# Kernel optimization log

Hardware: AMD Instinct MI355X
Metric: run time of the kernel (lower is better)

Reference implementation:

```python
import jax, jax.numpy as jnp
import numpy as np
from jax import lax

D_MODEL = 1000
D_INNER = 2000   # expand=2
D_STATE = 8
D_CONV = 4
DT_RANK = 63     # ceil(1000/16)
DIM_OUT = 64


def setup_inputs() -> dict:
    key = jax.random.key(0)
    ks = jax.random.split(key, 16)
    s = 0.02
    x = jax.random.normal(ks[0], (8, 2048, D_MODEL), dtype=jnp.float32)
    params = {
        'w_norm': jnp.ones((D_MODEL,), jnp.float32),
        'W_in':   jax.random.normal(ks[1], (D_MODEL, 2 * D_INNER)) * s,
        'conv_w': jax.random.normal(ks[2], (D_INNER, D_CONV)) * s,
        'conv_b': jnp.zeros((D_INNER,), jnp.float32),
        'W_xproj': jax.random.normal(ks[3], (D_INNER, DT_RANK + 2 * D_STATE)) * s,
        'W_dt':   jax.random.normal(ks[4], (DT_RANK, D_INNER)) * s,
        'b_dt':   jax.random.normal(ks[5], (D_INNER,)) * s,
        'A_log':  jnp.broadcast_to(jnp.log(jnp.arange(1, D_STATE + 1, dtype=jnp.float32)), (D_INNER, D_STATE)).copy(),
        'Dp':     jnp.ones((D_INNER,), jnp.float32),
        'W_outp': jax.random.normal(ks[6], (D_INNER, D_MODEL)) * s,
        'W_fc':   jax.random.normal(ks[7], (D_MODEL, D_MODEL)) * s,
        'b_fc':   jnp.zeros((D_MODEL,), jnp.float32),
        'W_mu':   jax.random.normal(ks[8], (D_MODEL, DIM_OUT)) * s,
        'b_mu':   jnp.zeros((DIM_OUT,), jnp.float32),
        'W_sig':  jax.random.normal(ks[9], (D_MODEL, DIM_OUT)) * s,
        'b_sig':  jnp.zeros((DIM_OUT,), jnp.float32),
    }
    return {'x': x, **params}


def _rmsnorm(x, w, eps=1e-5):
    var = jnp.mean(x * x, axis=-1, keepdims=True)
    return x * lax.rsqrt(var + eps) * w


def _silu(x):
    return x * jax.nn.sigmoid(x)


def _mamba_block(x, w_norm, W_in, conv_w, conv_b, W_xproj, W_dt, b_dt, A_log, Dp, W_outp):
    B, L, _ = x.shape
    xn = _rmsnorm(x, w_norm)
    xz = xn @ W_in                                   # [B,L,2*ED]
    xc, z = jnp.split(xz, 2, axis=-1)                # each [B,L,ED]
    # depthwise causal conv1d
    xt = xc.transpose(0, 2, 1)                        # [B,ED,L]
    xt = lax.conv_general_dilated(
        xt, conv_w[:, None, :],                       # [ED,1,K]
        window_strides=(1,), padding=[(D_CONV - 1, 0)],
        feature_group_count=D_INNER,
        dimension_numbers=('NCH', 'OIH', 'NCH'))
    xc = xt.transpose(0, 2, 1) + conv_b               # [B,L,ED]
    xc = _silu(xc)
    dbc = xc @ W_xproj                                # [B,L,dt_rank+2N]
    dt, Bm, Cm = jnp.split(dbc, [DT_RANK, DT_RANK + D_STATE], axis=-1)
    delta = jax.nn.softplus(dt @ W_dt + b_dt)         # [B,L,ED]
    A = -jnp.exp(A_log)                               # [ED,N]

    def step(h, inp):
        x_t, d_t, B_t, C_t = inp                      # [B,ED],[B,ED],[B,N],[B,N]
        dA = jnp.exp(d_t[:, :, None] * A)             # [B,ED,N]
        h = dA * h + (d_t[:, :, None] * B_t[:, None, :]) * x_t[:, :, None]
        y = jnp.einsum('ben,bn->be', h, C_t)
        return h, y

    h0 = jnp.zeros((B, D_INNER, D_STATE), xc.dtype)
    xs = (xc.transpose(1, 0, 2), delta.transpose(1, 0, 2),
          Bm.transpose(1, 0, 2), Cm.transpose(1, 0, 2))
    _, ys = lax.scan(step, h0, xs)                    # [L,B,ED]
    y = ys.transpose(1, 0, 2) + Dp * xc               # [B,L,ED]
    y = y * _silu(z)
    return x + y @ W_outp                             # residual


def reference(x, w_norm, W_in, conv_w, conv_b, W_xproj, W_dt, b_dt, A_log, Dp,
              W_outp, W_fc, b_fc, W_mu, b_mu, W_sig, b_sig):
    e = _mamba_block(x, w_norm, W_in, conv_w, conv_b, W_xproj, W_dt, b_dt,
                     A_log, Dp, W_outp)
    e = e.mean(axis=1)                                # [B,d_model]; dropout=eval->identity
    h = jax.nn.elu(jnp.tanh(e @ W_fc + b_fc))
    mu = h @ W_mu + b_mu
    sigma = jax.nn.elu(h @ W_sig + b_sig) + 1.0 + 1e-14
    return (h, mu, sigma)
```

## Files before the change

kernel.cpp:

```cpp
#include <hip/hip_runtime.h>

#define DM    1000
#define DMP   1024
#define ED    2000
#define EDP   2048
#define NST   8
#define LSEQ  2048
#define NB    8
#define MTOT  16384
#define N1    4096
#define K1    1024
#define CHK   16
#define CLEN  (LSEQ/CHK)
#define MXCH  32

typedef unsigned short u16;
typedef __attribute__((ext_vector_type(4))) float f32x4;
typedef __attribute__((ext_vector_type(8))) short bf16x8;

__device__ __forceinline__ u16 f2bf(float f) {
    union { float f; unsigned u; } v; v.f = f;
    unsigned r = v.u + 0x7FFFu + ((v.u >> 16) & 1u);
    return (u16)(r >> 16);
}
__device__ __forceinline__ float bf2f(u16 h) {
    union { unsigned u; float f; } v; v.u = ((unsigned)h) << 16; return v.f;
}
__device__ __forceinline__ float siluf(float x) { return x / (1.f + __expf(-x)); }

__global__ void meanx_part(const float* __restrict__ x, float* __restrict__ part) {
    const int d = blockIdx.x * 256 + threadIdx.x;
    const int b = blockIdx.y;
    const int c = blockIdx.z;
    float s = 0.f;
    if (d < DM) {
        const int l0 = c * (LSEQ / MXCH);
        for (int l = l0; l < l0 + LSEQ / MXCH; ++l)
            s += x[((size_t)b * LSEQ + l) * DM + d];
    }
    part[(size_t)(b * MXCH + c) * DMP + d] = s;
}
__global__ void meanx_red(const float* __restrict__ part, float* __restrict__ xm) {
    const int d = blockIdx.x * 256 + threadIdx.x;
    const int b = blockIdx.y;
    float s = 0.f;
    #pragma unroll
    for (int c = 0; c < MXCH; ++c) s += part[(size_t)(b * MXCH + c) * DMP + d];
    xm[b * DMP + d] = s * (1.f / LSEQ);
}

__global__ void rms_kernel(const float* __restrict__ x, const float* __restrict__ w,
                           u16* __restrict__ xn) {
    const int row = blockIdx.x;
    const int tid = threadIdx.x;
    const float* xr = x + (size_t)row * DM;
    float ss = 0.f;
    for (int i = tid; i < DM; i += 256) { float v = xr[i]; ss = fmaf(v, v, ss); }
    #pragma unroll
    for (int o = 32; o > 0; o >>= 1) ss += __shfl_xor(ss, o);
    __shared__ float red[4];
    if ((tid & 63) == 0) red[tid >> 6] = ss;
    __syncthreads();
    float tot = red[0] + red[1] + red[2] + red[3];
    float sc = rsqrtf(tot * (1.f / DM) + 1e-5f);
    for (int i = tid; i < DMP; i += 256)
        xn[(size_t)row * DMP + i] = (i < DM) ? f2bf(xr[i] * sc * w[i]) : (u16)0;
}

__global__ void packWt_kernel(const float* __restrict__ W, u16* __restrict__ Wt) {
    __shared__ float t[32][33];
    int nt = blockIdx.x * 32, kt = blockIdx.y * 32;
    int tx = threadIdx.x, ty = threadIdx.y;
    for (int j = 0; j < 32; j += 8) {
        int k = kt + ty + j, n = nt + tx;
        t[ty + j][tx] = (k < DM && n < 2 * ED) ? W[(size_t)k * (2 * ED) + n] : 0.f;
    }
    __syncthreads();
    for (int j = 0; j < 32; j += 8) {
        int n = nt + ty + j, k = kt + tx;
        Wt[(size_t)n * K1 + k] = f2bf(t[tx][ty + j]);
    }
}
__global__ void packWxT_kernel(const float* __restrict__ W, u16* __restrict__ WxT) {
    int gid = blockIdx.x * 256 + threadIdx.x;
    int n = gid >> 11, k = gid & (EDP - 1);
    int c = (n < 63) ? n : ((n >= 64 && n < 80) ? n - 1 : -1);
    float v = (c >= 0 && k < ED) ? W[(size_t)k * 79 + c] : 0.f;
    WxT[gid] = f2bf(v);
}
__global__ void packWdtT_kernel(const float* __restrict__ W, u16* __restrict__ Wt) {
    int gid = blockIdx.x * 256 + threadIdx.x;
    int n = gid >> 6, k = gid & 63;
    float v = (n < ED && k < 63) ? W[(size_t)k * ED + n] : 0.f;
    Wt[gid] = f2bf(v);
}

template<int MODE>
__global__ __launch_bounds__(256, 2)
void gemm_bt(const u16* __restrict__ A, const u16* __restrict__ Bt,
             int lda, int ldb, int ksteps,
             u16* __restrict__ o0, u16* __restrict__ o1,
             float* __restrict__ of, const float* __restrict__ bias) {
    __shared__ u16 As[128 * 32];
    __shared__ u16 Bs[128 * 32];
    const int tid = threadIdx.x;
    const int wv = tid >> 6, ln = tid & 63;
    const int mbase = blockIdx.y << 7, nbase = blockIdx.x << 7;
    const int wm = (wv >> 1) << 6, wn = (wv & 1) << 6;
    const int fr = ln & 15, fo = ln >> 4;

    f32x4 acc[4][4];
    #pragma unroll
    for (int i = 0; i < 4; ++i)
        #pragma unroll
        for (int j = 0; j < 4; ++j) acc[i][j] = (f32x4){0.f, 0.f, 0.f, 0.f};

    for (int ks = 0; ks < ksteps; ++ks) {
        const int kt = ks << 5;
        __syncthreads();
        #pragma unroll
        for (int i = 0; i < 2; ++i) {
            int c = (wv << 7) + (i << 6) + ln;
            const u16* ga = A + (size_t)(mbase + (c >> 2)) * lda + kt + ((c & 3) << 3);
            __builtin_amdgcn_global_load_lds(
                (const __attribute__((address_space(1))) void*)ga,
                (__attribute__((address_space(3))) void*)&As[((wv << 7) + (i << 6)) * 8],
                16, 0, 0);
            const u16* gb = Bt + (size_t)(nbase + (c >> 2)) * ldb + kt + ((c & 3) << 3);
            __builtin_amdgcn_global_load_lds(
                (const __attribute__((address_space(1))) void*)gb,
                (__attribute__((address_space(3))) void*)&Bs[((wv << 7) + (i << 6)) * 8],
                16, 0, 0);
        }
        asm volatile("s_waitcnt vmcnt(0)" ::: "memory");
        __syncthreads();

        bf16x8 af[4], bg[4];
        #pragma unroll
        for (int i = 0; i < 4; ++i) {
            af[i] = *(const bf16x8*)&As[((wm + (i << 4) + fr) << 5) + (fo << 3)];
            bg[i] = *(const bf16x8*)&Bs[((wn + (i << 4) + fr) << 5) + (fo << 3)];
        }
        #pragma unroll
        for (int i = 0; i < 4; ++i)
            #pragma unroll
            for (int j = 0; j < 4; ++j)
                acc[i][j] = __builtin_amdgcn_mfma_f32_16x16x32_bf16(af[i], bg[j], acc[i][j], 0, 0, 0);
    }

    #pragma unroll
    for (int i = 0; i < 4; ++i) {
        #pragma unroll
        for (int j = 0; j < 4; ++j) {
            int col = nbase + wn + (j << 4) + fr;
            #pragma unroll
            for (int r = 0; r < 4; ++r) {
                int row = mbase + wm + (i << 4) + (fo << 2) + r;
                float v = acc[i][j][r];
                if (MODE == 0) {
                    if (col < ED)            o0[(size_t)row * EDP + col] = f2bf(v);
                    else if (col < 2 * ED)   o1[(size_t)row * EDP + (col - ED)] = f2bf(siluf(v));
                } else if (MODE == 1) {
                    if (col < 64)            o0[(size_t)row * 64 + col] = f2bf(v);
                    else if (col < 80)       of[(size_t)row * 16 + (col - 64)] = v;
                } else {
                    if (col < ED) {
                        float s = v + bias[col];
                        float sp = (s > 20.f) ? s : log1pf(__expf(s));
                        o0[(size_t)row * EDP + col] = f2bf(sp);
                    }
                }
            }
        }
    }
}

__global__ void conv_kernel(const u16* __restrict__ xcr, const float* __restrict__ cw,
                            const float* __restrict__ cb, u16* __restrict__ xca) {
    const int ed = blockIdx.x * 256 + threadIdx.x;
    const int row = blockIdx.y;
    if (ed >= ED) { xca[(size_t)row * EDP + ed] = 0; return; }
    const int l = row & (LSEQ - 1);
    const float4 w = ((const float4*)cw)[ed];
    float s = cb[ed];
    const float wj[4] = {w.x, w.y, w.z, w.w};
    #pragma unroll
    for (int j = 0; j < 4; ++j) {
        int lj = l - 3 + j;
        if (lj >= 0) s = fmaf(wj[j], bf2f(xcr[(size_t)(row - 3 + j) * EDP + ed]), s);
    }
    xca[(size_t)row * EDP + ed] = f2bf(siluf(s));
}

__global__ void scan1_kernel(const u16* __restrict__ dlt, const u16* __restrict__ xca,
                             const u16* __restrict__ zs, const float* __restrict__ bc,
                             const float* __restrict__ A_log, const float* __restrict__ Dp,
                             float* __restrict__ Pb, float* __restrict__ wb,
                             float* __restrict__ hlb, float* __restrict__ accb) {
    const int ed = blockIdx.x * 256 + threadIdx.x;
    const int b = blockIdx.y;
    const int c = blockIdx.z;
    const int edc = (ed < ED) ? ed : (ED - 1);
    float An[NST];
    #pragma unroll
    for (int n = 0; n < NST; ++n) An[n] = -__expf(A_log[edc * NST + n]);
    const float dpv = Dp[edc];
    float g[NST], cd[NST], w[NST];
    #pragma unroll
    for (int n = 0; n < NST; ++n) { g[n] = 0.f; cd[n] = 1.f; w[n] = 0.f; }
    float acc = 0.f;

    const size_t rbase = (size_t)b * LSEQ + (size_t)c * CLEN;
    const float4* bc4 = (const float4*)bc;
    size_t i0 = rbase * EDP + ed;
    float dv = bf2f(dlt[i0]), xv = bf2f(xca[i0]), zv = bf2f(zs[i0]);
    float4 q0 = bc4[rbase * 4 + 0], q1 = bc4[rbase * 4 + 1];
    float4 q2 = bc4[rbase * 4 + 2], q3 = bc4[rbase * 4 + 3];

    for (int l = 0; l < CLEN; ++l) {
        float dv2 = 0.f, xv2 = 0.f, zv2 = 0.f;
        float4 p0 = make_float4(0.f,0.f,0.f,0.f), p1 = p0, p2 = p0, p3 = p0;
        if (l + 1 < CLEN) {
            size_t i2 = (rbase + l + 1) * EDP + ed;
            dv2 = bf2f(dlt[i2]); xv2 = bf2f(xca[i2]); zv2 = bf2f(zs[i2]);
            p0 = bc4[(rbase + l + 1) * 4 + 0]; p1 = bc4[(rbase + l + 1) * 4 + 1];
            p2 = bc4[(rbase + l + 1) * 4 + 2]; p3 = bc4[(rbase + l + 1) * 4 + 3];
        }
        const float Bv[8] = {q0.x,q0.y,q0.z,q0.w,q1.x,q1.y,q1.z,q1.w};
        const float Cv[8] = {q2.x,q2.y,q2.z,q2.w,q3.x,q3.y,q3.z,q3.w};
        float dx = dv * xv;
        float yl = 0.f;
        #pragma unroll
        for (int n = 0; n < NST; ++n) {
            float dA = __expf(dv * An[n]);
            cd[n] *= dA;
            g[n] = fmaf(g[n], dA, dx * Bv[n]);
            yl = fmaf(g[n], Cv[n], yl);
            w[n] = fmaf(zv * Cv[n], cd[n], w[n]);
        }
        acc = fmaf(yl + dpv * xv, zv, acc);
        dv = dv2; xv = xv2; zv = zv2; q0 = p0; q1 = p1; q2 = p2; q3 = p3;
    }
    const size_t o = ((size_t)(b * CHK + c) * NST) * EDP + ed;
    #pragma unroll
    for (int n = 0; n < NST; ++n) {
        Pb [o + (size_t)n * EDP] = cd[n];
        wb [o + (size_t)n * EDP] = w[n];
        hlb[o + (size_t)n * EDP] = g[n];
    }
    accb[(size_t)(b * CHK + c) * EDP + ed] = acc;
}

__global__ void scan2_kernel(const float* __restrict__ Pb, const float* __restrict__ wb,
                             const float* __restrict__ hlb, const float* __restrict__ accb,
                             float* __restrict__ sy) {
    const int ed = blockIdx.x * 256 + threadIdx.x;
    const int b = blockIdx.y;
    float h[NST];
    #pragma unroll
    for (int n = 0; n < NST; ++n) h[n] = 0.f;
    float acc = 0.f;
    #pragma unroll
    for (int c = 0; c < CHK; ++c) {
        const size_t o = ((size_t)(b * CHK + c) * NST) * EDP + ed;
        acc += accb[(size_t)(b * CHK + c) * EDP + ed];
        #pragma unroll
        for (int n = 0; n < NST; ++n) acc = fmaf(wb[o + (size_t)n * EDP], h[n], acc);
        #pragma unroll
        for (int n = 0; n < NST; ++n)
            h[n] = fmaf(Pb[o + (size_t)n * EDP], h[n], hlb[o + (size_t)n * EDP]);
    }
    if (ed < ED) sy[b * EDP + ed] = acc * (1.f / LSEQ);
}

__global__ void e_part(const float* __restrict__ sy, const float* __restrict__ Wo,
                       float* __restrict__ ep) {
    const int d = blockIdx.x * 256 + threadIdx.x;
    const int b = blockIdx.y;
    const int kc = blockIdx.z;
    if (d >= DM) return;
    float s = 0.f;
    const int k0 = kc * 250;
    for (int k = k0; k < k0 + 250; ++k)
        s = fmaf(sy[b * EDP + k], Wo[(size_t)k * DM + d], s);
    ep[(size_t)(b * 8 + kc) * DMP + d] = s;
}
__global__ void e_red(const float* __restrict__ ep, const float* __restrict__ xm,
                      float* __restrict__ e) {
    const int d = blockIdx.x * 256 + threadIdx.x;
    const int b = blockIdx.y;
    if (d >= DM) return;
    float s = xm[b * DMP + d];
    #pragma unroll
    for (int kc = 0; kc < 8; ++kc) s += ep[(size_t)(b * 8 + kc) * DMP + d];
    e[b * DMP + d] = s;
}

__global__ void fc_part(const float* __restrict__ e, const float* __restrict__ Wfc,
                        float* __restrict__ fp) {
    const int d = blockIdx.x * 256 + threadIdx.x;
    const int b = blockIdx.y;
    const int kc = blockIdx.z;
    if (d >= DM) return;
    float s = 0.f;
    const int k0 = kc * 250;
    for (int k = k0; k < k0 + 250; ++k)
        s = fmaf(e[b * DMP + k], Wfc[(size_t)k * DM + d], s);
    fp[(size_t)(b * 4 + kc) * DMP + d] = s;
}
__global__ void fc_red(const float* __restrict__ fp, const float* __restrict__ bfc,
                       float* __restrict__ out) {
    const int d = blockIdx.x * 256 + threadIdx.x;
    const int b = blockIdx.y;
    if (d >= DM) return;
    float s = bfc[d];
    #pragma unroll
    for (int kc = 0; kc < 4; ++kc) s += fp[(size_t)(b * 4 + kc) * DMP + d];
    float t = tanhf(s);
    out[b * DM + d] = (t > 0.f) ? t : expm1f(t);
}

__global__ void head_part(const float* __restrict__ hout, const float* __restrict__ Wmu,
                          const float* __restrict__ Wsig, float* __restrict__ hp) {
    const int o = threadIdx.x;
    const int b = blockIdx.x;
    const int kc = blockIdx.y;
    float sm = 0.f, sg = 0.f;
    const int k0 = kc * 125;
    for (int k = k0; k < k0 + 125; ++k) {
        float hv = hout[b * DM + k];
        sm = fmaf(hv, Wmu[k * 64 + o], sm);
        sg = fmaf(hv, Wsig[k * 64 + o], sg);
    }
    hp[(size_t)(b * 8 + kc) * 128 + o]      = sm;
    hp[(size_t)(b * 8 + kc) * 128 + 64 + o] = sg;
}
__global__ void head_red(const float* __restrict__ hp, const float* __restrict__ bmu,
                         const float* __restrict__ bsig, float* __restrict__ out) {
    const int o = threadIdx.x;
    const int b = blockIdx.x;
    float sm = bmu[o], sg = bsig[o];
    #pragma unroll
    for (int kc = 0; kc < 8; ++kc) {
        sm += hp[(size_t)(b * 8 + kc) * 128 + o];
        sg += hp[(size_t)(b * 8 + kc) * 128 + 64 + o];
    }
    out[8000 + b * 64 + o] = sm;
    float el = (sg > 0.f) ? sg : expm1f(sg);
    out[8512 + b * 64 + o] = el + 1.f + 1e-14f;
}

extern "C" void kernel_launch(void* const* d_in, const int* in_sizes, int n_in,
                              void* d_out, int out_size, void* d_ws, size_t ws_size,
                              hipStream_t stream) {
    const float* x       = (const float*)d_in[0];
    const float* w_norm  = (const float*)d_in[1];
    const float* W_in    = (const float*)d_in[2];
    const float* conv_w  = (const float*)d_in[3];
    const float* conv_b  = (const float*)d_in[4];
    const float* W_xproj = (const float*)d_in[5];
    const float* W_dt    = (const float*)d_in[6];
    const float* b_dt    = (const float*)d_in[7];
    const float* A_log   = (const float*)d_in[8];
    const float* Dp      = (const float*)d_in[9];
    const float* W_outp  = (const float*)d_in[10];
    const float* W_fc    = (const float*)d_in[11];
    const float* b_fc    = (const float*)d_in[12];
    const float* W_mu    = (const float*)d_in[13];
    const float* b_mu    = (const float*)d_in[14];
    const float* W_sig   = (const float*)d_in[15];
    const float* b_sig   = (const float*)d_in[16];
    float* out = (float*)d_out;

    char* p = (char*)d_ws;
    auto al = [](size_t b) { return (b + 255) & ~(size_t)255; };
    auto carve = [&](size_t bytes) { char* r = p; p += al(bytes); return r; };

    u16*   Wt    = (u16*)carve((size_t)N1 * K1 * 2);
    u16*   WxT   = (u16*)carve((size_t)128 * EDP * 2);
    u16*   WdtT  = (u16*)carve((size_t)EDP * 64 * 2);
    float* syb   = (float*)carve((size_t)NB * EDP * 4);
    float* xmb   = (float*)carve((size_t)NB * DMP * 4);
    float* eb    = (float*)carve((size_t)NB * DMP * 4);
    float* mpart = (float*)carve((size_t)NB * MXCH * DMP * 4);
    float* ep    = (float*)carve((size_t)NB * 8 * DMP * 4);
    float* fp    = (float*)carve((size_t)NB * 4 * DMP * 4);
    float* hp    = (float*)carve((size_t)NB * 8 * 128 * 4);

    size_t used = (size_t)(p - (char*)d_ws);
    size_t unit = al((size_t)LSEQ * DMP * 2) + 3 * al((size_t)LSEQ * EDP * 2)
                + al((size_t)LSEQ * 64 * 2) + al((size_t)LSEQ * 16 * 4);
    size_t avail = (ws_size > used) ? ws_size - used : 0;
    int g = 8;
    while (g > 1 && (size_t)g * unit > avail) g >>= 1;
    const int M = g * LSEQ;

    char*  reg0 = carve((size_t)M * DMP * 2);
    char*  reg1 = carve((size_t)M * EDP * 2);
    u16*   zsb  = (u16*)carve((size_t)M * EDP * 2);
    u16*   xca  = (u16*)carve((size_t)M * EDP * 2);
    u16*   dtb  = (u16*)carve((size_t)M * 64 * 2);
    float* bcb  = (float*)carve((size_t)M * 16 * 4);

    u16*   xn   = (u16*)reg0;
    const size_t MB1 = (size_t)1 << 20;
    float* Pb   = (float*)reg0;
    float* wbuf = (float*)(reg0 + (size_t)g * MB1);
    float* hlb  = (float*)(reg0 + (size_t)2 * g * MB1);
    float* accb = (float*)(reg0 + (size_t)3 * g * MB1);
    u16*   xcr  = (u16*)reg1;
    u16*   dlt  = (u16*)reg1;

    meanx_part <<<dim3(4, NB, MXCH), 256, 0, stream>>>(x, mpart);
    meanx_red  <<<dim3(4, NB), 256, 0, stream>>>(mpart, xmb);
    packWt_kernel<<<dim3(128, 32), dim3(32, 8), 0, stream>>>(W_in, Wt);
    packWxT_kernel<<<1024, 256, 0, stream>>>(W_xproj, WxT);
    packWdtT_kernel<<<512, 256, 0, stream>>>(W_dt, WdtT);

    for (int b0 = 0; b0 < NB; b0 += g) {
        const float* xg = x + (size_t)b0 * LSEQ * DM;
        rms_kernel <<<M, 256, 0, stream>>>(xg, w_norm, xn);
        gemm_bt<0><<<dim3(N1 / 128, M / 128), 256, 0, stream>>>(xn, Wt, K1, K1, K1 / 32,
                                                                xcr, zsb, nullptr, nullptr);
        conv_kernel<<<dim3(EDP / 256, M), 256, 0, stream>>>(xcr, conv_w, conv_b, xca);
        gemm_bt<1><<<dim3(1, M / 128), 256, 0, stream>>>(xca, WxT, EDP, EDP, EDP / 32,
                                                         dtb, nullptr, bcb, nullptr);
        gemm_bt<2><<<dim3(EDP / 128, M / 128), 256, 0, stream>>>(dtb, WdtT, 64, 64, 2,
                                                                 dlt, nullptr, nullptr, b_dt);
        scan1_kernel<<<dim3(EDP / 256, g, CHK), 256, 0, stream>>>(dlt, xca, zsb, bcb,
                                                                  A_log, Dp, Pb, wbuf, hlb, accb);
        scan2_kernel<<<dim3(EDP / 256, g), 256, 0, stream>>>(Pb, wbuf, hlb, accb,
                                                             syb + (size_t)b0 * EDP);
    }

    e_part <<<dim3(4, NB, 8), 256, 0, stream>>>(syb, W_outp, ep);
    e_red  <<<dim3(4, NB), 256, 0, stream>>>(ep, xmb, eb);
    fc_part<<<dim3(4, NB, 4), 256, 0, stream>>>(eb, W_fc, fp);
    fc_red <<<dim3(4, NB), 256, 0, stream>>>(fp, b_fc, out);
    head_part<<<dim3(NB, 8), 64, 0, stream>>>(out, W_mu, W_sig, hp);
    head_red <<<NB, 64, 0, stream>>>(hp, b_mu, b_sig, out);
}
```

Measured before the change: 931.8 us.

## Vectorize elementwise kernels, swizzle GEMM block order, batch tail matvecs

Switches meanx_part, rms_kernel and conv_kernel to float4 and bf16x8 vectorized loads and stores. Conv now processes 8 channels per thread with one block per row. The GEMM block index is remapped with a stride-8 swizzle to change L2 reuse. The tail matvec kernels (e_part, fc_part, head_part) now process all 8 batches per thread, so each weight element is read once, with K-split counts adjusted. Together these aim to cut memory traffic and instruction count, at the cost of fewer threads in the tail kernels.

Result: no change. 921.1 us (-1.2%).

```diff
diff --git a/kernel.cpp b/kernel.cpp
--- a/kernel.cpp
+++ b/kernel.cpp
@@ -17,6 +17,7 @@
 typedef unsigned short u16;
 typedef __attribute__((ext_vector_type(4))) float f32x4;
 typedef __attribute__((ext_vector_type(8))) short bf16x8;
+typedef __attribute__((ext_vector_type(4))) unsigned short u16x4;
 
 __device__ __forceinline__ u16 f2bf(float f) {
     union { float f; unsigned u; } v; v.f = f;
@@ -29,16 +30,18 @@
 __device__ __forceinline__ float siluf(float x) { return x / (1.f + __expf(-x)); }
 
 __global__ void meanx_part(const float* __restrict__ x, float* __restrict__ part) {
-    const int d = blockIdx.x * 256 + threadIdx.x;
+    const int t = threadIdx.x;
     const int b = blockIdx.y;
     const int c = blockIdx.z;
-    float s = 0.f;
-    if (d < DM) {
+    float4 s = make_float4(0.f, 0.f, 0.f, 0.f);
+    if (t < 250) {
         const int l0 = c * (LSEQ / MXCH);
-        for (int l = l0; l < l0 + LSEQ / MXCH; ++l)
-            s += x[((size_t)b * LSEQ + l) * DM + d];
-    }
-    part[(size_t)(b * MXCH + c) * DMP + d] = s;
+        for (int l = l0; l < l0 + LSEQ / MXCH; ++l) {
+            float4 v = ((const float4*)(x + ((size_t)b * LSEQ + l) * DM))[t];
+            s.x += v.x; s.y += v.y; s.z += v.z; s.w += v.w;
+        }
+    }
+    ((float4*)(part + (size_t)(b * MXCH + c) * DMP))[t] = s;
 }
 __global__ void meanx_red(const float* __restrict__ part, float* __restrict__ xm) {
     const int d = blockIdx.x * 256 + threadIdx.x;
@@ -55,7 +58,10 @@
     const int tid = threadIdx.x;
     const float* xr = x + (size_t)row * DM;
     float ss = 0.f;
-    for (int i = tid; i < DM; i += 256) { float v = xr[i]; ss = fmaf(v, v, ss); }
+    if (tid < 250) {
+        float4 v = ((const float4*)xr)[tid];
+        ss = v.x * v.x + v.y * v.y + v.z * v.z + v.w * v.w;
+    }
     #pragma unroll
     for (int o = 32; o > 0; o >>= 1) ss += __shfl_xor(ss, o);
     __shared__ float red[4];
@@ -63,8 +69,14 @@
     __syncthreads();
     float tot = red[0] + red[1] + red[2] + red[3];
     float sc = rsqrtf(tot * (1.f / DM) + 1e-5f);
-    for (int i = tid; i < DMP; i += 256)
-        xn[(size_t)row * DMP + i] = (i < DM) ? f2bf(xr[i] * sc * w[i]) : (u16)0;
+    u16x4 o4 = (u16x4){0, 0, 0, 0};
+    if (tid < 250) {
+        float4 v = ((const float4*)xr)[tid];
+        float4 g = ((const float4*)w)[tid];
+        o4[0] = f2bf(v.x * sc * g.x); o4[1] = f2bf(v.y * sc * g.y);
+        o4[2] = f2bf(v.z * sc * g.z); o4[3] = f2bf(v.w * sc * g.w);
+    }
+    *(u16x4*)&xn[(size_t)row * DMP + 4 * tid] = o4;
 }
 
 __global__ void packWt_kernel(const float* __restrict__ W, u16* __restrict__ Wt) {
@@ -105,7 +117,10 @@
     __shared__ u16 Bs[128 * 32];
     const int tid = threadIdx.x;
     const int wv = tid >> 6, ln = tid & 63;
-    const int mbase = blockIdx.y << 7, nbase = blockIdx.x << 7;
+    const int nwg = gridDim.x * gridDim.y;
+    const int fid = blockIdx.y * gridDim.x + blockIdx.x;
+    const int sw  = ((fid & 7) * (nwg >> 3)) + (fid >> 3);
+    const int mbase = (sw / gridDim.x) << 7, nbase = (sw % gridDim.x) << 7;
     const int wm = (wv >> 1) << 6, wn = (wv & 1) << 6;
     const int fr = ln & 15, fo = ln >> 4;
 
@@ -177,19 +192,40 @@
 
 __global__ void conv_kernel(const u16* __restrict__ xcr, const float* __restrict__ cw,
                             const float* __restrict__ cb, u16* __restrict__ xca) {
-    const int ed = blockIdx.x * 256 + threadIdx.x;
-    const int row = blockIdx.y;
-    if (ed >= ED) { xca[(size_t)row * EDP + ed] = 0; return; }
+    const int e8 = threadIdx.x;
+    const int row = blockIdx.x;
+    const int ed0 = e8 * 8;
+    const size_t base = (size_t)row * EDP + ed0;
+    if (ed0 >= ED) {
+        *(bf16x8*)&xca[base] = (bf16x8){0, 0, 0, 0, 0, 0, 0, 0};
+        return;
+    }
     const int l = row & (LSEQ - 1);
-    const float4 w = ((const float4*)cw)[ed];
-    float s = cb[ed];
-    const float wj[4] = {w.x, w.y, w.z, w.w};
+    float wv[8][4], acc[8];
+    #pragma unroll
+    for (int t = 0; t < 8; ++t) {
+        float4 q = ((const float4*)cw)[ed0 + t];
+        wv[t][0] = q.x; wv[t][1] = q.y; wv[t][2] = q.z; wv[t][3] = q.w;
+    }
+    {
+        float4 b0 = ((const float4*)cb)[e8 * 2];
+        float4 b1 = ((const float4*)cb)[e8 * 2 + 1];
+        acc[0] = b0.x; acc[1] = b0.y; acc[2] = b0.z; acc[3] = b0.w;
+        acc[4] = b1.x; acc[5] = b1.y; acc[6] = b1.z; acc[7] = b1.w;
+    }
     #pragma unroll
     for (int j = 0; j < 4; ++j) {
-        int lj = l - 3 + j;
-        if (lj >= 0) s = fmaf(wj[j], bf2f(xcr[(size_t)(row - 3 + j) * EDP + ed]), s);
-    }
-    xca[(size_t)row * EDP + ed] = f2bf(siluf(s));
+        if (l - 3 + j >= 0) {
+            bf16x8 r = *(const bf16x8*)&xcr[(size_t)(row - 3 + j) * EDP + ed0];
+            #pragma unroll
+            for (int t = 0; t < 8; ++t)
+                acc[t] = fmaf(wv[t][j], bf2f((u16)r[t]), acc[t]);
+        }
+    }
+    bf16x8 o;
+    #pragma unroll
+    for (int t = 0; t < 8; ++t) o[t] = (short)f2bf(siluf(acc[t]));
+    *(bf16x8*)&xca[base] = o;
 }
 
 __global__ void scan1_kernel(const u16* __restrict__ dlt, const u16* __restrict__ xca,
@@ -276,14 +312,19 @@
 __global__ void e_part(const float* __restrict__ sy, const float* __restrict__ Wo,
                        float* __restrict__ ep) {
     const int d = blockIdx.x * 256 + threadIdx.x;
-    const int b = blockIdx.y;
-    const int kc = blockIdx.z;
+    const int kc = blockIdx.y;
     if (d >= DM) return;
-    float s = 0.f;
-    const int k0 = kc * 250;
-    for (int k = k0; k < k0 + 250; ++k)
-        s = fmaf(sy[b * EDP + k], Wo[(size_t)k * DM + d], s);
-    ep[(size_t)(b * 8 + kc) * DMP + d] = s;
+    float s[NB];
+    #pragma unroll
+    for (int b = 0; b < NB; ++b) s[b] = 0.f;
+    const int k0 = kc * 125;
+    for (int k = k0; k < k0 + 125; ++k) {
+        float wv = Wo[(size_t)k * DM + d];
+        #pragma unroll
+        for (int b = 0; b < NB; ++b) s[b] = fmaf(sy[b * EDP + k], wv, s[b]);
+    }
+    #pragma unroll
+    for (int b = 0; b < NB; ++b) ep[(size_t)(b * 16 + kc) * DMP + d] = s[b];
 }
 __global__ void e_red(const float* __restrict__ ep, const float* __restrict__ xm,
                       float* __restrict__ e) {
@@ -292,21 +333,26 @@
     if (d >= DM) return;
     float s = xm[b * DMP + d];
     #pragma unroll
-    for (int kc = 0; kc < 8; ++kc) s += ep[(size_t)(b * 8 + kc) * DMP + d];
+    for (int kc = 0; kc < 16; ++kc) s += ep[(size_t)(b * 16 + kc) * DMP + d];
     e[b * DMP + d] = s;
 }
 
 __global__ void fc_part(const float* __restrict__ e, const float* __restrict__ Wfc,
                         float* __restrict__ fp) {
     const int d = blockIdx.x * 256 + threadIdx.x;
-    const int b = blockIdx.y;
-    const int kc = blockIdx.z;
+    const int kc = blockIdx.y;
     if (d >= DM) return;
-    float s = 0.f;
-    const int k0 = kc * 250;
-    for (int k = k0; k < k0 + 250; ++k)
-        s = fmaf(e[b * DMP + k], Wfc[(size_t)k * DM + d], s);
-    fp[(size_t)(b * 4 + kc) * DMP + d] = s;
+    float s[NB];
+    #pragma unroll
+    for (int b = 0; b < NB; ++b) s[b] = 0.f;
+    const int k0 = kc * 125;
+    for (int k = k0; k < k0 + 125; ++k) {
+        float wv = Wfc[(size_t)k * DM + d];
+        #pragma unroll
+        for (int b = 0; b < NB; ++b) s[b] = fmaf(e[b * DMP + k], wv, s[b]);
+    }
+    #pragma unroll
+    for (int b = 0; b < NB; ++b) fp[(size_t)(b * 8 + kc) * DMP + d] = s[b];
 }
 __global__ void fc_red(const float* __restrict__ fp, const float* __restrict__ bfc,
                        float* __restrict__ out) {
@@ -315,7 +361,7 @@
     if (d >= DM) return;
     float s = bfc[d];
     #pragma unroll
-    for (int kc = 0; kc < 4; ++kc) s += fp[(size_t)(b * 4 + kc) * DMP + d];
+    for (int kc = 0; kc < 8; ++kc) s += fp[(size_t)(b * 8 + kc) * DMP + d];
     float t = tanhf(s);
     out[b * DM + d] = (t > 0.f) ? t : expm1f(t);
 }
@@ -323,17 +369,25 @@
 __global__ void head_part(const float* __restrict__ hout, const float* __restrict__ Wmu,
                           const float* __restrict__ Wsig, float* __restrict__ hp) {
     const int o = threadIdx.x;
-    const int b = blockIdx.x;
-    const int kc = blockIdx.y;
-    float sm = 0.f, sg = 0.f;
+    const int kc = blockIdx.x;
+    float sm[NB], sg[NB];
+    #pragma unroll
+    for (int b = 0; b < NB; ++b) { sm[b] = 0.f; sg[b] = 0.f; }
     const int k0 = kc * 125;
     for (int k = k0; k < k0 + 125; ++k) {
-        float hv = hout[b * DM + k];
-        sm = fmaf(hv, Wmu[k * 64 + o], sm);
-        sg = fmaf(hv, Wsig[k * 64 + o], sg);
-    }
-    hp[(size_t)(b * 8 + kc) * 128 + o]      = sm;
-    hp[(size_t)(b * 8 + kc) * 128 + 64 + o] = sg;
+        float wm = Wmu[k * 64 + o], ws = Wsig[k * 64 + o];
+        #pragma unroll
+        for (int b = 0; b < NB; ++b) {
+            float hv = hout[b * DM + k];
+            sm[b] = fmaf(hv, wm, sm[b]);
+            sg[b] = fmaf(hv, ws, sg[b]);
+        }
+    }
+    #pragma unroll
+    for (int b = 0; b < NB; ++b) {
+        hp[(size_t)(b * 8 + kc) * 128 + o]      = sm[b];
+        hp[(size_t)(b * 8 + kc) * 128 + 64 + o] = sg[b];
+    }
 }
 __global__ void head_red(const float* __restrict__ hp, const float* __restrict__ bmu,
                          const float* __restrict__ bsig, float* __restrict__ out) {
@@ -383,8 +437,8 @@
     float* xmb   = (float*)carve((size_t)NB * DMP * 4);
     float* eb    = (float*)carve((size_t)NB * DMP * 4);
     float* mpart = (float*)carve((size_t)NB * MXCH * DMP * 4);
-    float* ep    = (float*)carve((size_t)NB * 8 * DMP * 4);
-    float* fp    = (float*)carve((size_t)NB * 4 * DMP * 4);
+    float* ep    = (float*)carve((size_t)NB * 16 * DMP * 4);
+    float* fp    = (float*)carve((size_t)NB * 8 * DMP * 4);
     float* hp    = (float*)carve((size_t)NB * 8 * 128 * 4);
 
     size_t used = (size_t)(p - (char*)d_ws);
@@ -411,7 +465,7 @@
     u16*   xcr  = (u16*)reg1;
     u16*   dlt  = (u16*)reg1;
 
-    meanx_part <<<dim3(4, NB, MXCH), 256, 0, stream>>>(x, mpart);
+    meanx_part <<<dim3(1, NB, MXCH), 256, 0, stream>>>(x, mpart);
     meanx_red  <<<dim3(4, NB), 256, 0, stream>>>(mpart, xmb);
     packWt_kernel<<<dim3(128, 32), dim3(32, 8), 0, stream>>>(W_in, Wt);
     packWxT_kernel<<<1024, 256, 0, stream>>>(W_xproj, WxT);
@@ -422,7 +476,7 @@
         rms_kernel <<<M, 256, 0, stream>>>(xg, w_norm, xn);
         gemm_bt<0><<<dim3(N1 / 128, M / 128), 256, 0, stream>>>(xn, Wt, K1, K1, K1 / 32,
                                                                 xcr, zsb, nullptr, nullptr);
-        conv_kernel<<<dim3(EDP / 256, M), 256, 0, stream>>>(xcr, conv_w, conv_b, xca);
+        conv_kernel<<<M, 256, 0, stream>>>(xcr, conv_w, conv_b, xca);
         gemm_bt<1><<<dim3(1, M / 128), 256, 0, stream>>>(xca, WxT, EDP, EDP, EDP / 32,
                                                          dtb, nullptr, bcb, nullptr);
         gemm_bt<2><<<dim3(EDP / 128, M / 128), 256, 0, stream>>>(dtb, WdtT, 64, 64, 2,
@@ -433,10 +487,10 @@
                                                              syb + (size_t)b0 * EDP);
     }
 
-    e_part <<<dim3(4, NB, 8), 256, 0, stream>>>(syb, W_outp, ep);
+    e_part <<<dim3(4, 16), 256, 0, stream>>>(syb, W_outp, ep);
     e_red  <<<dim3(4, NB), 256, 0, stream>>>(ep, xmb, eb);
-    fc_part<<<dim3(4, NB, 4), 256, 0, stream>>>(eb, W_fc, fp);
+    fc_part<<<dim3(4, 8), 256, 0, stream>>>(eb, W_fc, fp);
     fc_red <<<dim3(4, NB), 256, 0, stream>>>(fp, b_fc, out);
-    head_part<<<dim3(NB, 8), 64, 0, stream>>>(out, W_mu, W_sig, hp);
+    head_part<<<8, 64, 0, stream>>>(out, W_mu, W_sig, hp);
     head_red <<<NB, 64, 0, stream>>>(hp, b_mu, b_sig, out);
 }
```
